# Optimization experiments

Measured on AMD Instinct MI355X. Metric: run time of the kernel, lower is better.

The kernel has to match this reference:

```python
import jax, jax.numpy as jnp
import numpy as np

B, G, D, H, L, MLP = 64, 512, 384, 6, 12, 4
DH = D // H
MASK_RATIO = 0.6
KEEP_RATIO = 0.1
PAD_VAL = -1.0
START_VAL = 1.0
POS_HID = 128
NEG = -1e9


def setup_inputs() -> dict:
    key = jax.random.key(0)
    ks = jax.random.split(key, 24)
    s = 0.02
    inp = {
        "x": jax.random.normal(ks[0], (B, G, D), jnp.float32),
        "center_points": jax.random.normal(ks[1], (B, G, 3), jnp.float32),
        "mask_noise": jax.random.uniform(ks[2], (B, G), jnp.float32),
        # pos embedder MLP: 3 -> 128 -> D
        "pos_w1": jax.random.normal(ks[3], (3, POS_HID), jnp.float32) * s,
        "pos_b1": jnp.zeros((POS_HID,), jnp.float32),
        "pos_w2": jax.random.normal(ks[4], (POS_HID, D), jnp.float32) * s,
        "pos_b2": jnp.zeros((D,), jnp.float32),
        # stacked per-layer transformer params
        "ln1_w": jnp.ones((L, D), jnp.float32),
        "ln1_b": jnp.zeros((L, D), jnp.float32),
        "qkv_w": jax.random.normal(ks[5], (L, D, 3 * D), jnp.float32) * s,
        "qkv_b": jnp.zeros((L, 3 * D), jnp.float32),
        "proj_w": jax.random.normal(ks[6], (L, D, D), jnp.float32) * s,
        "proj_b": jnp.zeros((L, D), jnp.float32),
        "ln2_w": jnp.ones((L, D), jnp.float32),
        "ln2_b": jnp.zeros((L, D), jnp.float32),
        "fc1_w": jax.random.normal(ks[7], (L, D, MLP * D), jnp.float32) * s,
        "fc1_b": jnp.zeros((L, MLP * D), jnp.float32),
        "fc2_w": jax.random.normal(ks[8], (L, MLP * D, D), jnp.float32) * s,
        "fc2_b": jnp.zeros((L, D), jnp.float32),
        # final LayerNorm
        "norm_w": jnp.ones((D,), jnp.float32),
        "norm_b": jnp.zeros((D,), jnp.float32),
    }
    return inp


def _layer_norm(h, w, b, eps=1e-5):
    mu = jnp.mean(h, axis=-1, keepdims=True)
    var = jnp.mean(jnp.square(h - mu), axis=-1, keepdims=True)
    return (h - mu) * jax.lax.rsqrt(var + eps) * w + b


def _random_mask(center, noise):
    # padding tokens: all coords equal PAD_VAL
    pad = jnp.all(center == PAD_VAL, axis=-1)                      # [B, G] bool
    if MASK_RATIO == 0:
        return jnp.zeros(pad.shape, bool), pad
    n = (G - jnp.sum(pad.astype(jnp.int32), axis=-1))              # non-padding count
    k = (n.astype(jnp.float32) * KEEP_RATIO).astype(jnp.int32)     # kept-first tokens
    m = ((n - k).astype(jnp.float32) * MASK_RATIO).astype(jnp.int32)
    M = jnp.max(m)
    j = jnp.arange(G)[None, :]
    # shuffle region [k, n): pick m random slots (uniform subset via rank of noise)
    region = (j >= k[:, None]) & (j < n[:, None])
    u = jnp.where(region, noise, jnp.inf)
    rank = jnp.argsort(jnp.argsort(u, axis=-1), axis=-1)
    shuf = (rank < m[:, None]) & region
    # tail of ones: positions [n, n + M - m)
    tail = (j >= n[:, None]) & (j < (n + M - m)[:, None])
    return shuf | tail, pad


def _attention(h, qw, qb, pw, pb, bias):
    qkv = (h @ qw + qb).reshape(B, G, 3, H, DH).transpose(2, 0, 3, 1, 4)
    q, k, v = qkv[0], qkv[1], qkv[2]                               # [B, H, G, DH]
    s = jnp.einsum('bhqd,bhkd->bhqk', q, k) * (DH ** -0.5) + bias
    a = jax.nn.softmax(s, axis=-1)
    o = jnp.einsum('bhqk,bhkd->bhqd', a, v).transpose(0, 2, 1, 3).reshape(B, G, D)
    return o @ pw + pb


def _forward(x, center_points, mask_noise,
             pos_w1, pos_b1, pos_w2, pos_b2,
             ln1_w, ln1_b, qkv_w, qkv_b, proj_w, proj_b,
             ln2_w, ln2_b, fc1_w, fc1_b, fc2_w, fc2_b,
             norm_w, norm_b):
    # shift right + start token
    start = jnp.full((B, 1, D), START_VAL, x.dtype)
    x = jnp.concatenate([start, x[:, :-1, :]], axis=1)
    # positional embedding of shifted centers + start-token pos
    pos = jax.nn.gelu(center_points[:, :-1, :] @ pos_w1 + pos_b1, approximate=False) @ pos_w2 + pos_b2
    pos = jnp.concatenate([jnp.full((B, 1, D), START_VAL, x.dtype), pos], axis=1)
    # causal | (random column mask & ~eye) attention mask
    triu = jnp.triu(jnp.ones((G, G), bool), 1)
    rand_mask, pad = _random_mask(center_points, mask_noise)
    eye = jnp.eye(G, dtype=bool)
    attn_mask = triu[None, :, :] | (rand_mask[:, None, :] & ~eye[None, :, :])   # [B, G, G]
    bias = jnp.where(attn_mask | pad[:, None, :], NEG, 0.0)[:, None, :, :]      # [B,1,G,G]

    def block(h, p):
        l1w, l1b, qw, qb, pw, pb, l2w, l2b, f1w, f1b, f2w, f2b = p
        h = h + pos
        h = h + _attention(_layer_norm(h, l1w, l1b), qw, qb, pw, pb, bias)
        h = h + (jax.nn.gelu(_layer_norm(h, l2w, l2b) @ f1w + f1b, approximate=False) @ f2w + f2b)
        return h, None

    x, _ = jax.lax.scan(block, x, (ln1_w, ln1_b, qkv_w, qkv_b, proj_w, proj_b,
                                   ln2_w, ln2_b, fc1_w, fc1_b, fc2_w, fc2_b))
    x = _layer_norm(x, norm_w, norm_b)
    return x, pad, attn_mask


def reference(x, center_points, mask_noise,
              pos_w1, pos_b1, pos_w2, pos_b2,
              ln1_w, ln1_b, qkv_w, qkv_b, proj_w, proj_b,
              ln2_w, ln2_b, fc1_w, fc1_b, fc2_w, fc2_b,
              norm_w, norm_b):
    out, pad, attn_mask = _forward(x, center_points, mask_noise,
                                   pos_w1, pos_b1, pos_w2, pos_b2,
                                   ln1_w, ln1_b, qkv_w, qkv_b, proj_w, proj_b,
                                   ln2_w, ln2_b, fc1_w, fc1_b, fc2_w, fc2_b,
                                   norm_w, norm_b)
    # torch repeat_interleave over heads -> [B*H, G, G]
    return out, pad, jnp.repeat(attn_mask, H, axis=0)
```

## Files before the change

kernel.cpp:

```cpp
#include <hip/hip_runtime.h>
#include <math.h>

typedef _Float16 f16;
typedef f16 f16x8 __attribute__((ext_vector_type(8)));
typedef f16 f16v2 __attribute__((ext_vector_type(2)));
typedef float f32x4 __attribute__((ext_vector_type(4)));

#define NB 64
#define NG 512
#define ND 384
#define NH 6
#define NL 12
#define NDH 64
#define BG (NB * NG)
#define BGD (BG * ND)

#define OFF_WQKV   0
#define OFF_WPROJ  2654208
#define OFF_WFC1   3538944
#define OFF_WFC2   7077888
#define OFF_FLAGS  10616832
#define OFF_NKM    10625024
#define OFF_MMAX   10625216
#define OFF_POS    10625280
#define OFF_HID    23208192
#define OFF_Y      25305344
#define OFF_YBIG   31596800
#define OFF_QB     56762624
#define OFF_KB     63054080
#define OFF_VT     69345536
#define OFF_OB     75636992
#define OFF_W2T    81928448
#define OFF_HB     81953024

typedef __attribute__((address_space(3))) void lds_t;
typedef const __attribute__((address_space(1))) void gmem_t;
__device__ __forceinline__ void gload16(const void* g, void* l)
{
    __builtin_amdgcn_global_load_lds((gmem_t*)g, (lds_t*)l, 16, 0, 0);
}

__global__ __launch_bounds__(256)
void transpose_kernel(const float* __restrict__ src, f16* __restrict__ dst,
                      int K, int N)
{
    __shared__ float tile[32][33];
    const int l = blockIdx.z;
    const float* S = src + (size_t)l * K * N;
    f16* D = dst + (size_t)l * K * N;
    const int n0 = blockIdx.x * 32, k0 = blockIdx.y * 32;
    const int tx = threadIdx.x, ty = threadIdx.y;
#pragma unroll
    for (int i = 0; i < 32; i += 8)
        tile[ty + i][tx] = S[(size_t)(k0 + ty + i) * N + n0 + tx];
    __syncthreads();
#pragma unroll
    for (int i = 0; i < 32; i += 8)
        D[(size_t)(n0 + ty + i) * K + k0 + tx] = (f16)tile[tx][ty + i];
}

__global__ __launch_bounds__(256)
void dpos_a(const float* cen, const float* w1, const float* b1, f16* hid)
{
    const int idx = blockIdx.x * 256 + threadIdx.x;
    if (idx >= BG * 128) return;
    const int t = idx >> 7, k = idx & 127;
    const int g = t & (NG - 1);
    if (g == 0) { hid[idx] = (f16)0.f; return; }
    const float* c = cen + (size_t)(t - 1) * 3;
    const float hv = c[0] * w1[k] + c[1] * w1[128 + k] + c[2] * w1[256 + k] + b1[k];
    hid[idx] = (f16)(0.5f * hv * (1.0f + erff(hv * 0.70710678118654752f)));
}

__global__ __launch_bounds__(384)
void pos_fix(float* pos)
{
    const int b = blockIdx.x;
    pos[((size_t)b * NG) * ND + threadIdx.x] = 1.0f;
}

__global__ __launch_bounds__(512)
void dmask_a(const float* cen, float* pad_out, int* nkm)
{
    const int b = blockIdx.x, j = threadIdx.x;
    const float* c = cen + ((size_t)b * NG + j) * 3;
    const bool pad = (c[0] == -1.f) && (c[1] == -1.f) && (c[2] == -1.f);
    pad_out[b * NG + j] = pad ? 1.f : 0.f;
    if (j == 0) {
        int cnt = 0;
        for (int i = 0; i < NG; i++) {
            const float* ci = cen + ((size_t)b * NG + i) * 3;
            cnt += (ci[0] == -1.f && ci[1] == -1.f && ci[2] == -1.f) ? 1 : 0;
        }
        const int n = NG - cnt;
        const int k = (int)((float)n * 0.1f);
        const int m = (int)((float)(n - k) * 0.6f);
        nkm[b * 3] = n; nkm[b * 3 + 1] = k; nkm[b * 3 + 2] = m;
    }
}

__global__ void dmask_m(const int* nkm, int* Mmax)
{
    if (threadIdx.x == 0 && blockIdx.x == 0) {
        int M = 0;
        for (int b = 0; b < NB; b++) M = max(M, nkm[b * 3 + 2]);
        *Mmax = M;
    }
}

__global__ __launch_bounds__(512)
void dmask_b(const float* cen, const float* noi, const int* nkm,
             const int* Mmax, unsigned char* flags)
{
    const int b = blockIdx.x, j = threadIdx.x;
    const int n = nkm[b * 3], k = nkm[b * 3 + 1], m = nkm[b * 3 + 2];
    const int M = *Mmax;
    const float nz = noi[b * NG + j];
    const bool inreg = (j >= k) && (j < n);
    bool shuf = false;
    if (inreg) {
        int cnt = 0;
        for (int i = 0; i < NG; i++) {
            if (i < k || i >= n) continue;
            const float ui = noi[b * NG + i];
            cnt += (ui < nz) || (ui == nz && i < j);
        }
        shuf = cnt < m;
    }
    const float* c = cen + ((size_t)b * NG + j) * 3;
    const bool pad = (c[0] == -1.f) && (c[1] == -1.f) && (c[2] == -1.f);
    const bool tail = (j >= n) && (j < n + M - m);
    flags[b * NG + j] = (unsigned char)(((shuf | tail) ? 1 : 0) | (pad ? 2 : 0));
}

__global__ __launch_bounds__(512)
void flags_rep_kernel(const unsigned char* flags, float* mo)
{
    const int bq = blockIdx.x;
    const int b = bq >> 9, q = bq & (NG - 1);
    const int j = threadIdx.x;
    mo[(((size_t)(b * NH) * NG + q) * NG) + j] = (float)flags[b * NG + j];
}

__global__ __launch_bounds__(512)
void mask_out_kernel(float* mo)
{
    const int bq = blockIdx.x;
    const int b = bq >> 9, q = bq & (NG - 1);
    const int j = threadIdx.x;
    const unsigned char f =
        (unsigned char)mo[(((size_t)(b * NH) * NG + q) * NG) + j];
    const float val = ((q < j) || ((f & 1) && (q != j))) ? 1.0f : 0.0f;
#pragma unroll
    for (int h = 0; h < NH; h++)
        mo[(((size_t)(b * NH + h) * NG + q) * NG) + j] = val;
}

__global__ __launch_bounds__(256)
void h0_kernel(const float* x, const float* pos, f16* h)
{
    const size_t i = (size_t)blockIdx.x * 256 + threadIdx.x;
    const int g = (int)((i / ND) & (NG - 1));
    const float xv = x[(g == 0) ? i : (i - ND)];
    const float base = (g == 0) ? 1.0f : xv;
    h[i] = (f16)(base + pos[i]);
}

template<int MODE>
__global__ __launch_bounds__(256)
void lnb_kernel(const f16* __restrict__ h,
                const float* __restrict__ w, const float* __restrict__ bb,
                f16* __restrict__ y16, float* __restrict__ y32)
{
    __shared__ float red[4][64];
    const int wid = threadIdx.x >> 6;
    const int lane = threadIdx.x & 63;
    const int t = blockIdx.x * 4 + wid;
    const size_t base = (size_t)t * ND + lane;
    float v[6];
    float s = 0.f;
#pragma unroll
    for (int i = 0; i < 6; i++) {
        const float xv = (float)h[base + i * 64];
        v[i] = xv; s += xv;
    }
    red[wid][lane] = s;
    __syncthreads();
    for (int st = 32; st > 0; st >>= 1) {
        if (lane < st) red[wid][lane] += red[wid][lane + st];
        __syncthreads();
    }
    const float mu = red[wid][0] * (1.f / ND);
    float vs = 0.f;
#pragma unroll
    for (int i = 0; i < 6; i++) { const float d = v[i] - mu; vs += d * d; }
    __syncthreads();
    red[wid][lane] = vs;
    __syncthreads();
    for (int st = 32; st > 0; st >>= 1) {
        if (lane < st) red[wid][lane] += red[wid][lane + st];
        __syncthreads();
    }
    const float rstd = rsqrtf(red[wid][0] * (1.f / ND) + 1e-5f);
#pragma unroll
    for (int i = 0; i < 6; i++) {
        const float o = (v[i] - mu) * rstd * w[lane + i * 64] + bb[lane + i * 64];
        if constexpr (MODE == 2) y32[base + i * 64] = o;
        else                     y16[base + i * 64] = (f16)o;
    }
}

template<int MODE>
__global__ __launch_bounds__(256)
void gemm_kernel(const f16* __restrict__ A, const f16* __restrict__ Bt,
                 const float* __restrict__ bias, int K, int NT,
                 f16* __restrict__ hres,
                 float* __restrict__ out32, f16* __restrict__ out16,
                 f16* __restrict__ Qo, f16* __restrict__ Ko, f16* __restrict__ Vo)
{
    __shared__ f16 sA[128 * 64];
    __shared__ f16 sB[128 * 64];
    const int tid = threadIdx.x;
    const int w = tid >> 6, lane = tid & 63;
    const int lr = lane & 15, lg = lane >> 4;
    const int wm = w >> 1, wn = w & 1;
    const int N = NT * 128;

    const int nwg = gridDim.x;
    const int chunk = nwg >> 3;
    const int flat = (blockIdx.x & 7) * chunk + (blockIdx.x >> 3);
    const int m0 = (flat / NT) * 128;
    const int n0 = (flat % NT) * 128;

    f32x4 acc[4][4];
#pragma unroll
    for (int mf = 0; mf < 4; mf++)
#pragma unroll
        for (int nf = 0; nf < 4; nf++)
            acc[mf][nf] = (f32x4){0.f, 0.f, 0.f, 0.f};

    const int srow0 = w * 8 + (lane >> 3);
    const int scolB = (lane & 7) * 16;

    for (int k0 = 0; k0 < K; k0 += 64) {
        __syncthreads();
#pragma unroll
        for (int i = 0; i < 4; i++) {
            const int row = i * 32 + srow0;
            const int colB = scolB ^ ((row & 7) << 4);
            const char* ga = (const char*)(A + (size_t)(m0 + row) * K + k0) + colB;
            const char* gb = (const char*)(Bt + (size_t)(n0 + row) * K + k0) + colB;
            gload16(ga, (char*)sA + row * 128 + scolB);
            gload16(gb, (char*)sB + row * 128 + scolB);
        }
        __syncthreads();
#pragma unroll
        for (int kk = 0; kk < 64; kk += 32) {
            f16x8 af[4], bf[4];
#pragma unroll
            for (int mf = 0; mf < 4; mf++) {
                const int r = wm * 64 + mf * 16 + lr;
                const int cb = ((kk + lg * 8) * 2) ^ ((r & 7) << 4);
                af[mf] = *(const f16x8*)((const char*)sA + r * 128 + cb);
            }
#pragma unroll
            for (int nf = 0; nf < 4; nf++) {
                const int r = wn * 64 + nf * 16 + lr;
                const int cb = ((kk + lg * 8) * 2) ^ ((r & 7) << 4);
                bf[nf] = *(const f16x8*)((const char*)sB + r * 128 + cb);
            }
#pragma unroll
            for (int mf = 0; mf < 4; mf++)
#pragma unroll
                for (int nf = 0; nf < 4; nf++)
                    acc[mf][nf] = __builtin_amdgcn_mfma_f32_16x16x32_f16(
                        af[mf], bf[nf], acc[mf][nf], 0, 0, 0);
        }
    }

#pragma unroll
    for (int mf = 0; mf < 4; mf++) {
#pragma unroll
        for (int nf = 0; nf < 4; nf++) {
            const int n_g = n0 + wn * 64 + nf * 16 + lr;
            const float bv = bias[n_g];
#pragma unroll
            for (int r = 0; r < 4; r++) {
                const int m_g = m0 + wm * 64 + mf * 16 + lg * 4 + r;
                const float v = acc[mf][nf][r] + bv;
                const size_t oidx = (size_t)m_g * N + n_g;
                if constexpr (MODE == 1) {
                    hres[oidx] = (f16)((float)hres[oidx] + v);
                } else if constexpr (MODE == 2) {
                    const float ge = 0.5f * v * (1.0f + erff(v * 0.70710678118654752f));
                    out16[oidx] = (f16)ge;
                } else if constexpr (MODE == 3) {
                    out32[oidx] = v;
                } else {
                    const int which = n_g / ND;
                    const int rem = n_g - which * ND;
                    const int hh = rem >> 6, dh = rem & 63;
                    const int bb2 = m_g >> 9, gg = m_g & (NG - 1);
                    if (which == 0)
                        Qo[((size_t)(bb2 * NH + hh) * NG + gg) * NDH + dh] = (f16)v;
                    else if (which == 1)
                        Ko[((size_t)(bb2 * NH + hh) * NG + gg) * NDH + dh] = (f16)v;
                    else
                        Vo[((size_t)(bb2 * NH + hh) * NDH + dh) * NG + gg] = (f16)v;
                }
            }
        }
    }
}

template<int ADDPOS>
__global__ __launch_bounds__(512)
void gemmln_kernel(const f16* __restrict__ A, const f16* __restrict__ Bt,
                   const float* __restrict__ bias, int K,
                   f16* __restrict__ hres, const float* __restrict__ posadd,
                   const float* __restrict__ lw, const float* __restrict__ lb,
                   f16* __restrict__ Y)
{
    __shared__ f16 sA[128 * 64];
    __shared__ f16 sB[384 * 64];
    __shared__ float part[2][128][2];
    const int tid = threadIdx.x;
    const int w = tid >> 6, lane = tid & 63;
    const int lr = lane & 15, lg = lane >> 4;
    const int wm = w >> 2, wn = w & 3;
    const int vm = w >> 1, vn = w & 1;

    const int nwg = gridDim.x;
    const int chunk = nwg >> 3;
    const int m0 = ((blockIdx.x & 7) * chunk + (blockIdx.x >> 3)) * 128;
    (void)wm; (void)wn;

    f32x4 acc[2][12];
#pragma unroll
    for (int mf = 0; mf < 2; mf++)
#pragma unroll
        for (int nf = 0; nf < 12; nf++)
            acc[mf][nf] = (f32x4){0.f, 0.f, 0.f, 0.f};

    const int srowA = tid >> 3;
    const int scolB = (tid & 7) * 16;

    for (int k0 = 0; k0 < K; k0 += 64) {
        __syncthreads();
#pragma unroll
        for (int i = 0; i < 2; i++) {
            const int row = i * 64 + srowA;
            const int colB = scolB ^ ((row & 7) << 4);
            gload16((const char*)(A + (size_t)(m0 + row) * K + k0) + colB,
                    (char*)sA + row * 128 + scolB);
        }
#pragma unroll
        for (int i = 0; i < 6; i++) {
            const int row = i * 64 + srowA;
            const int colB = scolB ^ ((row & 7) << 4);
            gload16((const char*)(Bt + (size_t)row * K + k0) + colB,
                    (char*)sB + row * 128 + scolB);
        }
        __syncthreads();
#pragma unroll
        for (int kk = 0; kk < 64; kk += 32) {
            f16x8 af[2];
#pragma unroll
            for (int mf = 0; mf < 2; mf++) {
                const int r = vm * 32 + mf * 16 + lr;
                const int cb = ((kk + lg * 8) * 2) ^ ((r & 7) << 4);
                af[mf] = *(const f16x8*)((const char*)sA + r * 128 + cb);
            }
#pragma unroll
            for (int half = 0; half < 2; half++) {
                f16x8 bf[6];
#pragma unroll
                for (int j = 0; j < 6; j++) {
                    const int nf = half * 6 + j;
                    const int r = vn * 192 + nf * 16 + lr;
                    const int cb = ((kk + lg * 8) * 2) ^ ((r & 7) << 4);
                    bf[j] = *(const f16x8*)((const char*)sB + r * 128 + cb);
                }
#pragma unroll
                for (int mf = 0; mf < 2; mf++)
#pragma unroll
                    for (int j = 0; j < 6; j++)
                        acc[mf][half * 6 + j] = __builtin_amdgcn_mfma_f32_16x16x32_f16(
                            af[mf], bf[j], acc[mf][half * 6 + j], 0, 0, 0);
            }
        }
    }

    f16v2 hn[2][12][2];
    float rs[2][4], rq[2][4];
#pragma unroll
    for (int mf = 0; mf < 2; mf++)
#pragma unroll
        for (int r = 0; r < 4; r++) { rs[mf][r] = 0.f; rq[mf][r] = 0.f; }

#pragma unroll
    for (int mf = 0; mf < 2; mf++) {
#pragma unroll
        for (int nf = 0; nf < 12; nf++) {
            const int col = vn * 192 + nf * 16 + lr;
            const float bv = bias[col];
#pragma unroll
            for (int r = 0; r < 4; r++) {
                const int row_g = m0 + vm * 32 + mf * 16 + lg * 4 + r;
                const size_t oidx = (size_t)row_g * ND + col;
                float hv = (float)hres[oidx] + acc[mf][nf][r] + bv;
                if constexpr (ADDPOS) hv += posadd[oidx];
                const f16 hf = (f16)hv;
                hn[mf][nf][r >> 1][r & 1] = hf;
                const float hff = (float)hf;
                rs[mf][r] += hff;
                rq[mf][r] += hff * hff;
            }
        }
    }
#pragma unroll
    for (int mf = 0; mf < 2; mf++)
#pragma unroll
        for (int r = 0; r < 4; r++) {
#pragma unroll
            for (int off = 1; off < 16; off <<= 1) {
                rs[mf][r] += __shfl_xor(rs[mf][r], off);
                rq[mf][r] += __shfl_xor(rq[mf][r], off);
            }
        }
    if (lr == 0) {
#pragma unroll
        for (int mf = 0; mf < 2; mf++)
#pragma unroll
            for (int r = 0; r < 4; r++) {
                const int rl = vm * 32 + mf * 16 + lg * 4 + r;
                part[vn][rl][0] = rs[mf][r];
                part[vn][rl][1] = rq[mf][r];
            }
    }
    __syncthreads();

    float mus[2][4], rstds[2][4];
#pragma unroll
    for (int mf = 0; mf < 2; mf++)
#pragma unroll
        for (int r = 0; r < 4; r++) {
            const int rl = vm * 32 + mf * 16 + lg * 4 + r;
            const float s = part[0][rl][0] + part[1][rl][0];
            const float q = part[0][rl][1] + part[1][rl][1];
            const float mu = s * (1.f / ND);
            const float var = q * (1.f / ND) - mu * mu;
            mus[mf][r] = mu;
            rstds[mf][r] = rsqrtf(var + 1e-5f);
        }

#pragma unroll
    for (int mf = 0; mf < 2; mf++) {
#pragma unroll
        for (int nf = 0; nf < 12; nf++) {
            const int col = vn * 192 + nf * 16 + lr;
            const float wl = lw[col];
            const float bl = lb[col];
#pragma unroll
            for (int r = 0; r < 4; r++) {
                const int row_g = m0 + vm * 32 + mf * 16 + lg * 4 + r;
                const size_t oidx = (size_t)row_g * ND + col;
                const f16 hf = hn[mf][nf][r >> 1][r & 1];
                hres[oidx] = hf;
                const float o = ((float)hf - mus[mf][r]) * rstds[mf][r] * wl + bl;
                Y[oidx] = (f16)o;
            }
        }
    }
}

__global__ __launch_bounds__(256)
void attn_kernel(const f16* __restrict__ Q, const f16* __restrict__ Kt,
                 const f16* __restrict__ V, const unsigned char* __restrict__ flags,
                 f16* __restrict__ O)
{
    __shared__ f16 sQ[128][72];
    __shared__ f16 sK[64][72];
    __shared__ f16 sV[64][72];
    __shared__ f16 sP[4][16][72];
    const int tid = threadIdx.x;
    const int w = tid >> 6, lane = tid & 63;
    const int lr = lane & 15, lg = lane >> 4;
    const int q0 = blockIdx.x * 128;
    const int bh = blockIdx.y;
    const int b = bh / NH, hh = bh - b * NH;
    const f16* Qg = Q + ((size_t)bh * NG + q0) * NDH;
    const f16* Kg = Kt + (size_t)bh * NG * NDH;
    const f16* Vg = V + (size_t)bh * NDH * NG;
    const unsigned char* fl = flags + b * NG;

#pragma unroll
    for (int i = 0; i < 4; i++) {
        const int c = tid + i * 256;
        const int r = c >> 3, cc = (c & 7) * 8;
        *(f16x8*)&sQ[r][cc] = *(const f16x8*)(Qg + r * NDH + cc);
    }
    __syncthreads();
    f16x8 aq[2][2];
#pragma unroll
    for (int hf = 0; hf < 2; hf++) {
        aq[hf][0] = *(const f16x8*)&sQ[hf * 64 + w * 16 + lr][lg * 8];
        aq[hf][1] = *(const f16x8*)&sQ[hf * 64 + w * 16 + lr][32 + lg * 8];
    }

    float m_run[2][4], l_run[2][4];
    f32x4 o[2][4];
#pragma unroll
    for (int hf = 0; hf < 2; hf++)
#pragma unroll
        for (int r = 0; r < 4; r++) {
            m_run[hf][r] = -INFINITY; l_run[hf][r] = 0.f;
            o[hf][r] = (f32x4){0.f, 0.f, 0.f, 0.f};
        }

    const int ntile = 2 * blockIdx.x + 2;
    for (int jt = 0; jt < ntile; jt++) {
        const int j0 = jt * 64;
        __syncthreads();
#pragma unroll
        for (int i = 0; i < 2; i++) {
            const int c = tid + i * 256;
            const int r = c >> 3, cc = (c & 7) * 8;
            *(f16x8*)&sK[r][cc] = *(const f16x8*)(Kg + (size_t)(j0 + r) * NDH + cc);
            *(f16x8*)&sV[r][cc] = *(const f16x8*)(Vg + (size_t)r * NG + j0 + cc);
        }
        __syncthreads();

#pragma unroll
        for (int hf = 0; hf < 2; hf++) {
            if (jt >= ntile - 1 + hf) continue;
            f32x4 s[4];
#pragma unroll
            for (int nf = 0; nf < 4; nf++) s[nf] = (f32x4){0.f, 0.f, 0.f, 0.f};
#pragma unroll
            for (int kf = 0; kf < 2; kf++) {
#pragma unroll
                for (int nf = 0; nf < 4; nf++) {
                    f16x8 bk = *(const f16x8*)&sK[nf * 16 + lr][kf * 32 + lg * 8];
                    s[nf] = __builtin_amdgcn_mfma_f32_16x16x32_f16(aq[hf][kf], bk, s[nf], 0, 0, 0);
                }
            }
#pragma unroll
            for (int nf = 0; nf < 4; nf++) {
                const int j_g = j0 + nf * 16 + lr;
                const unsigned char f = fl[j_g];
#pragma unroll
                for (int r = 0; r < 4; r++) {
                    const int q_g = q0 + hf * 64 + w * 16 + lg * 4 + r;
                    const bool masked = (q_g < j_g) || (f & 2) || ((f & 1) && (j_g != q_g));
                    s[nf][r] = s[nf][r] * 0.125f + (masked ? -1e9f : 0.f);
                }
            }
#pragma unroll
            for (int r = 0; r < 4; r++) {
                float mx = fmaxf(fmaxf(s[0][r], s[1][r]), fmaxf(s[2][r], s[3][r]));
#pragma unroll
                for (int off = 1; off < 16; off <<= 1) mx = fmaxf(mx, __shfl_xor(mx, off));
                const float nm = fmaxf(m_run[hf][r], mx);
                const float sc = __expf(m_run[hf][r] - nm);
                m_run[hf][r] = nm;
                l_run[hf][r] *= sc;
#pragma unroll
                for (int nf = 0; nf < 4; nf++) o[hf][nf][r] *= sc;
                float ls = 0.f;
#pragma unroll
                for (int nf = 0; nf < 4; nf++) {
                    const float p = __expf(s[nf][r] - nm);
                    ls += p;
                    sP[w][lg * 4 + r][nf * 16 + lr] = (f16)p;
                }
                l_run[hf][r] += ls;
            }
#pragma unroll
            for (int kf = 0; kf < 2; kf++) {
                f16x8 ap = *(const f16x8*)&sP[w][lr][kf * 32 + lg * 8];
#pragma unroll
                for (int nf = 0; nf < 4; nf++) {
                    f16x8 bv = *(const f16x8*)&sV[nf * 16 + lr][kf * 32 + lg * 8];
                    o[hf][nf] = __builtin_amdgcn_mfma_f32_16x16x32_f16(ap, bv, o[hf][nf], 0, 0, 0);
                }
            }
        }
    }

#pragma unroll
    for (int hf = 0; hf < 2; hf++) {
        float inv[4];
#pragma unroll
        for (int r = 0; r < 4; r++) {
            float l = l_run[hf][r];
#pragma unroll
            for (int off = 1; off < 16; off <<= 1) l += __shfl_xor(l, off);
            inv[r] = 1.f / l;
        }
#pragma unroll
        for (int nf = 0; nf < 4; nf++) {
#pragma unroll
            for (int r = 0; r < 4; r++) {
                const int q_g = q0 + hf * 64 + w * 16 + lg * 4 + r;
                const int dh = nf * 16 + lr;
                O[((size_t)(b * NG + q_g)) * ND + hh * NDH + dh] = (f16)(o[hf][nf][r] * inv[r]);
            }
        }
    }
}

extern "C" void kernel_launch(void* const* d_in, const int* in_sizes, int n_in,
                              void* d_out, int out_size, void* d_ws, size_t ws_size,
                              hipStream_t stream)
{
    (void)d_ws; (void)ws_size;

    static const int exp_sizes[21] = {
        12582912, 98304, 32768,
        384, 128, 49152, 384,
        4608, 4608,
        5308416, 13824,
        1769472, 4608,
        4608, 4608,
        7077888, 18432,
        7077888, 4608,
        384, 384
    };
    if (n_in != 21 || out_size != 113278976) return;
    for (int i = 0; i < 21; i++) if (in_sizes[i] != exp_sizes[i]) return;

    const float* x    = (const float*)d_in[0];
    const float* cen  = (const float*)d_in[1];
    const float* noi  = (const float*)d_in[2];
    const float* pw1  = (const float*)d_in[3];
    const float* pb1  = (const float*)d_in[4];
    const float* pw2  = (const float*)d_in[5];
    const float* pb2  = (const float*)d_in[6];
    const float* ln1w = (const float*)d_in[7];
    const float* ln1b = (const float*)d_in[8];
    const float* qkvw = (const float*)d_in[9];
    const float* qkvb = (const float*)d_in[10];
    const float* projw= (const float*)d_in[11];
    const float* projb= (const float*)d_in[12];
    const float* ln2w = (const float*)d_in[13];
    const float* ln2b = (const float*)d_in[14];
    const float* fc1w = (const float*)d_in[15];
    const float* fc1b = (const float*)d_in[16];
    const float* fc2w = (const float*)d_in[17];
    const float* fc2b = (const float*)d_in[18];
    const float* nw   = (const float*)d_in[19];
    const float* nb   = (const float*)d_in[20];

    float* out0    = (float*)d_out;
    float* pad_out = out0 + BGD;
    float* R       = pad_out + BG;

    f16* WqkvT  = (f16*)(R + OFF_WQKV);
    f16* WprojT = (f16*)(R + OFF_WPROJ);
    f16* Wfc1T  = (f16*)(R + OFF_WFC1);
    f16* Wfc2T  = (f16*)(R + OFF_WFC2);
    unsigned char* flags = (unsigned char*)(R + OFF_FLAGS);
    int* nkm  = (int*)(R + OFF_NKM);
    int* Mmax = (int*)(R + OFF_MMAX);
    float* POS = R + OFF_POS;
    f16* HID   = (f16*)(R + OFF_HID);
    f16* Y     = (f16*)(R + OFF_Y);
    f16* Ybig  = (f16*)(R + OFF_YBIG);
    f16* Qb    = (f16*)(R + OFF_QB);
    f16* Kb    = (f16*)(R + OFF_KB);
    f16* Vt    = (f16*)(R + OFF_VT);
    f16* Ob    = (f16*)(R + OFF_OB);
    f16* W2T   = (f16*)(R + OFF_W2T);
    f16* Hb    = (f16*)(R + OFF_HB);

    dim3 tb(32, 8);
    transpose_kernel<<<dim3(36, 12, NL), tb, 0, stream>>>(qkvw, WqkvT, 384, 1152);
    transpose_kernel<<<dim3(12, 12, NL), tb, 0, stream>>>(projw, WprojT, 384, 384);
    transpose_kernel<<<dim3(48, 12, NL), tb, 0, stream>>>(fc1w, Wfc1T, 384, 1536);
    transpose_kernel<<<dim3(12, 48, NL), tb, 0, stream>>>(fc2w, Wfc2T, 1536, 384);
    transpose_kernel<<<dim3(12, 4, 1),  tb, 0, stream>>>(pw2, W2T, 128, 384);

    dmask_a<<<NB, 512, 0, stream>>>(cen, pad_out, nkm);
    dmask_m<<<1, 64, 0, stream>>>(nkm, Mmax);
    dmask_b<<<NB, 512, 0, stream>>>(cen, noi, nkm, Mmax, flags);
    dpos_a<<<BG * 128 / 256, 256, 0, stream>>>(cen, pw1, pb1, HID);
    gemm_kernel<3><<<768, 256, 0, stream>>>(HID, W2T, pb2, 128, 3,
                                            nullptr, POS, nullptr,
                                            nullptr, nullptr, nullptr);
    pos_fix<<<NB, 384, 0, stream>>>(POS);
    h0_kernel<<<BGD / 256, 256, 0, stream>>>(x, POS, Hb);

    lnb_kernel<1><<<BG / 4, 256, 0, stream>>>(Hb, ln1w, ln1b, Y, nullptr);

    for (int l = 0; l < NL; l++) {
        gemm_kernel<0><<<2304, 256, 0, stream>>>(Y, WqkvT + (size_t)l * 442368,
                                                 qkvb + l * 1152, 384, 9,
                                                 nullptr, nullptr, nullptr,
                                                 Qb, Kb, Vt);
        attn_kernel<<<dim3(4, NB * NH), 256, 0, stream>>>(Qb, Kb, Vt, flags, Ob);
        gemmln_kernel<0><<<256, 512, 0, stream>>>(Ob, WprojT + (size_t)l * 147456,
                                                  projb + l * ND, 384,
                                                  Hb, nullptr,
                                                  ln2w + l * ND, ln2b + l * ND, Y);
        gemm_kernel<2><<<3072, 256, 0, stream>>>(Y, Wfc1T + (size_t)l * 589824,
                                                 fc1b + l * 1536, 384, 12,
                                                 nullptr, nullptr, Ybig,
                                                 nullptr, nullptr, nullptr);
        if (l < NL - 1) {
            gemmln_kernel<1><<<256, 512, 0, stream>>>(Ybig, Wfc2T + (size_t)l * 589824,
                                                      fc2b + l * ND, 1536,
                                                      Hb, POS,
                                                      ln1w + (l + 1) * ND, ln1b + (l + 1) * ND, Y);
        } else {
            gemm_kernel<1><<<768, 256, 0, stream>>>(Ybig, Wfc2T + (size_t)l * 589824,
                                                    fc2b + l * ND, 1536, 3,
                                                    Hb, nullptr, nullptr,
                                                    nullptr, nullptr, nullptr);
        }
    }

    lnb_kernel<2><<<BG / 4, 256, 0, stream>>>(Hb, nw, nb, nullptr, out0);
    flags_rep_kernel<<<BG, 512, 0, stream>>>(flags, R);
    mask_out_kernel<<<BG, 512, 0, stream>>>(R);
}
```

Before: 4.962 ms.

## Shrink attention query tile and read K/V directly; store positional embedding in fp16

The attention kernel now handles 64 queries per block instead of 128, launching twice as many blocks. It drops the shared-memory staging of Q, K and V and loads MFMA operands straight from global memory, removing the block barriers and the uneven two-half causal work split. Separately, the positional-embedding buffer is stored in fp16 rather than fp32, halving its write and its re-read in every fc2+LayerNorm epilogue. The trade-offs are lost K/V reuse through LDS, which means more global and L2 traffic from uncoalesced fragment loads, and lower precision on the positional add.

```diff
diff --git a/kernel.cpp b/kernel.cpp
--- a/kernel.cpp
+++ b/kernel.cpp
@@ -73,10 +73,10 @@
 }
 
 __global__ __launch_bounds__(384)
-void pos_fix(float* pos)
+void pos_fix(f16* pos)
 {
     const int b = blockIdx.x;
-    pos[((size_t)b * NG) * ND + threadIdx.x] = 1.0f;
+    pos[((size_t)b * NG) * ND + threadIdx.x] = (f16)1.0f;
 }
 
 __global__ __launch_bounds__(512)
@@ -157,13 +157,13 @@
 }
 
 __global__ __launch_bounds__(256)
-void h0_kernel(const float* x, const float* pos, f16* h)
+void h0_kernel(const float* x, const f16* pos, f16* h)
 {
     const size_t i = (size_t)blockIdx.x * 256 + threadIdx.x;
     const int g = (int)((i / ND) & (NG - 1));
     const float xv = x[(g == 0) ? i : (i - ND)];
     const float base = (g == 0) ? 1.0f : xv;
-    h[i] = (f16)(base + pos[i]);
+    h[i] = (f16)(base + (float)pos[i]);
 }
 
 template<int MODE>
@@ -214,8 +214,7 @@
 __global__ __launch_bounds__(256)
 void gemm_kernel(const f16* __restrict__ A, const f16* __restrict__ Bt,
                  const float* __restrict__ bias, int K, int NT,
-                 f16* __restrict__ hres,
-                 float* __restrict__ out32, f16* __restrict__ out16,
+                 f16* __restrict__ hres, f16* __restrict__ out16,
                  f16* __restrict__ Qo, f16* __restrict__ Ko, f16* __restrict__ Vo)
 {
     __shared__ f16 sA[128 * 64];
@@ -295,7 +294,7 @@
                     const float ge = 0.5f * v * (1.0f + erff(v * 0.70710678118654752f));
                     out16[oidx] = (f16)ge;
                 } else if constexpr (MODE == 3) {
-                    out32[oidx] = v;
+                    out16[oidx] = (f16)v;
                 } else {
                     const int which = n_g / ND;
                     const int rem = n_g - which * ND;
@@ -317,7 +316,7 @@
 __global__ __launch_bounds__(512)
 void gemmln_kernel(const f16* __restrict__ A, const f16* __restrict__ Bt,
                    const float* __restrict__ bias, int K,
-                   f16* __restrict__ hres, const float* __restrict__ posadd,
+                   f16* __restrict__ hres, const f16* __restrict__ posadd,
                    const float* __restrict__ lw, const float* __restrict__ lb,
                    f16* __restrict__ Y)
 {
@@ -327,13 +326,11 @@
     const int tid = threadIdx.x;
     const int w = tid >> 6, lane = tid & 63;
     const int lr = lane & 15, lg = lane >> 4;
-    const int wm = w >> 2, wn = w & 3;
     const int vm = w >> 1, vn = w & 1;
 
     const int nwg = gridDim.x;
     const int chunk = nwg >> 3;
     const int m0 = ((blockIdx.x & 7) * chunk + (blockIdx.x >> 3)) * 128;
-    (void)wm; (void)wn;
 
     f32x4 acc[2][12];
 #pragma unroll
@@ -409,7 +406,7 @@
                 const int row_g = m0 + vm * 32 + mf * 16 + lg * 4 + r;
                 const size_t oidx = (size_t)row_g * ND + col;
                 float hv = (float)hres[oidx] + acc[mf][nf][r] + bv;
-                if constexpr (ADDPOS) hv += posadd[oidx];
+                if constexpr (ADDPOS) hv += (float)posadd[oidx];
                 const f16 hf = (f16)hv;
                 hn[mf][nf][r >> 1][r & 1] = hf;
                 const float hff = (float)hf;
@@ -479,133 +476,104 @@
                  const f16* __restrict__ V, const unsigned char* __restrict__ flags,
                  f16* __restrict__ O)
 {
-    __shared__ f16 sQ[128][72];
-    __shared__ f16 sK[64][72];
-    __shared__ f16 sV[64][72];
     __shared__ f16 sP[4][16][72];
     const int tid = threadIdx.x;
     const int w = tid >> 6, lane = tid & 63;
     const int lr = lane & 15, lg = lane >> 4;
-    const int q0 = blockIdx.x * 128;
+    const int q0 = blockIdx.x * 64;
     const int bh = blockIdx.y;
     const int b = bh / NH, hh = bh - b * NH;
-    const f16* Qg = Q + ((size_t)bh * NG + q0) * NDH;
+    const f16* Qg = Q + (size_t)bh * NG * NDH;
     const f16* Kg = Kt + (size_t)bh * NG * NDH;
     const f16* Vg = V + (size_t)bh * NDH * NG;
     const unsigned char* fl = flags + b * NG;
 
-#pragma unroll
-    for (int i = 0; i < 4; i++) {
-        const int c = tid + i * 256;
-        const int r = c >> 3, cc = (c & 7) * 8;
-        *(f16x8*)&sQ[r][cc] = *(const f16x8*)(Qg + r * NDH + cc);
-    }
-    __syncthreads();
-    f16x8 aq[2][2];
-#pragma unroll
-    for (int hf = 0; hf < 2; hf++) {
-        aq[hf][0] = *(const f16x8*)&sQ[hf * 64 + w * 16 + lr][lg * 8];
-        aq[hf][1] = *(const f16x8*)&sQ[hf * 64 + w * 16 + lr][32 + lg * 8];
-    }
-
-    float m_run[2][4], l_run[2][4];
-    f32x4 o[2][4];
-#pragma unroll
-    for (int hf = 0; hf < 2; hf++)
-#pragma unroll
-        for (int r = 0; r < 4; r++) {
-            m_run[hf][r] = -INFINITY; l_run[hf][r] = 0.f;
-            o[hf][r] = (f32x4){0.f, 0.f, 0.f, 0.f};
-        }
-
-    const int ntile = 2 * blockIdx.x + 2;
+    const int qrow = q0 + w * 16 + lr;
+    f16x8 aq[2];
+    aq[0] = *(const f16x8*)(Qg + (size_t)qrow * NDH + lg * 8);
+    aq[1] = *(const f16x8*)(Qg + (size_t)qrow * NDH + 32 + lg * 8);
+
+    float m_run[4], l_run[4];
+    f32x4 o[4];
+#pragma unroll
+    for (int r = 0; r < 4; r++) { m_run[r] = -INFINITY; l_run[r] = 0.f; }
+#pragma unroll
+    for (int nf = 0; nf < 4; nf++) o[nf] = (f32x4){0.f, 0.f, 0.f, 0.f};
+
+    const int ntile = blockIdx.x + 1;
     for (int jt = 0; jt < ntile; jt++) {
         const int j0 = jt * 64;
-        __syncthreads();
-#pragma unroll
-        for (int i = 0; i < 2; i++) {
-            const int c = tid + i * 256;
-            const int r = c >> 3, cc = (c & 7) * 8;
-            *(f16x8*)&sK[r][cc] = *(const f16x8*)(Kg + (size_t)(j0 + r) * NDH + cc);
-            *(f16x8*)&sV[r][cc] = *(const f16x8*)(Vg + (size_t)r * NG + j0 + cc);
-        }
-        __syncthreads();
-
-#pragma unroll
-        for (int hf = 0; hf < 2; hf++) {
-            if (jt >= ntile - 1 + hf) continue;
-            f32x4 s[4];
-#pragma unroll
-            for (int nf = 0; nf < 4; nf++) s[nf] = (f32x4){0.f, 0.f, 0.f, 0.f};
-#pragma unroll
-            for (int kf = 0; kf < 2; kf++) {
-#pragma unroll
-                for (int nf = 0; nf < 4; nf++) {
-                    f16x8 bk = *(const f16x8*)&sK[nf * 16 + lr][kf * 32 + lg * 8];
-                    s[nf] = __builtin_amdgcn_mfma_f32_16x16x32_f16(aq[hf][kf], bk, s[nf], 0, 0, 0);
-                }
-            }
+
+        f32x4 s[4];
+#pragma unroll
+        for (int nf = 0; nf < 4; nf++) s[nf] = (f32x4){0.f, 0.f, 0.f, 0.f};
+#pragma unroll
+        for (int kf = 0; kf < 2; kf++) {
 #pragma unroll
             for (int nf = 0; nf < 4; nf++) {
-                const int j_g = j0 + nf * 16 + lr;
-                const unsigned char f = fl[j_g];
-#pragma unroll
-                for (int r = 0; r < 4; r++) {
-                    const int q_g = q0 + hf * 64 + w * 16 + lg * 4 + r;
-                    const bool masked = (q_g < j_g) || (f & 2) || ((f & 1) && (j_g != q_g));
-                    s[nf][r] = s[nf][r] * 0.125f + (masked ? -1e9f : 0.f);
-                }
-            }
+                f16x8 bk = *(const f16x8*)(Kg + (size_t)(j0 + nf * 16 + lr) * NDH
+                                           + kf * 32 + lg * 8);
+                s[nf] = __builtin_amdgcn_mfma_f32_16x16x32_f16(aq[kf], bk, s[nf], 0, 0, 0);
+            }
+        }
+#pragma unroll
+        for (int nf = 0; nf < 4; nf++) {
+            const int j_g = j0 + nf * 16 + lr;
+            const unsigned char f = fl[j_g];
 #pragma unroll
             for (int r = 0; r < 4; r++) {
-                float mx = fmaxf(fmaxf(s[0][r], s[1][r]), fmaxf(s[2][r], s[3][r]));
-#pragma unroll
-                for (int off = 1; off < 16; off <<= 1) mx = fmaxf(mx, __shfl_xor(mx, off));
-                const float nm = fmaxf(m_run[hf][r], mx);
-                const float sc = __expf(m_run[hf][r] - nm);
-                m_run[hf][r] = nm;
-                l_run[hf][r] *= sc;
-#pragma unroll
-                for (int nf = 0; nf < 4; nf++) o[hf][nf][r] *= sc;
-                float ls = 0.f;
-#pragma unroll
-                for (int nf = 0; nf < 4; nf++) {
-                    const float p = __expf(s[nf][r] - nm);
-                    ls += p;
-                    sP[w][lg * 4 + r][nf * 16 + lr] = (f16)p;
-                }
-                l_run[hf][r] += ls;
-            }
-#pragma unroll
-            for (int kf = 0; kf < 2; kf++) {
-                f16x8 ap = *(const f16x8*)&sP[w][lr][kf * 32 + lg * 8];
-#pragma unroll
-                for (int nf = 0; nf < 4; nf++) {
-                    f16x8 bv = *(const f16x8*)&sV[nf * 16 + lr][kf * 32 + lg * 8];
-                    o[hf][nf] = __builtin_amdgcn_mfma_f32_16x16x32_f16(ap, bv, o[hf][nf], 0, 0, 0);
-                }
-            }
-        }
-    }
-
-#pragma unroll
-    for (int hf = 0; hf < 2; hf++) {
-        float inv[4];
+                const int q_g = q0 + w * 16 + lg * 4 + r;
+                const bool masked = (q_g < j_g) || (f & 2) || ((f & 1) && (j_g != q_g));
+                s[nf][r] = s[nf][r] * 0.125f + (masked ? -1e9f : 0.f);
+            }
+        }
 #pragma unroll
         for (int r = 0; r < 4; r++) {
-            float l = l_run[hf][r];
-#pragma unroll
-            for (int off = 1; off < 16; off <<= 1) l += __shfl_xor(l, off);
-            inv[r] = 1.f / l;
-        }
-#pragma unroll
-        for (int nf = 0; nf < 4; nf++) {
-#pragma unroll
-            for (int r = 0; r < 4; r++) {
-                const int q_g = q0 + hf * 64 + w * 16 + lg * 4 + r;
-                const int dh = nf * 16 + lr;
-                O[((size_t)(b * NG + q_g)) * ND + hh * NDH + dh] = (f16)(o[hf][nf][r] * inv[r]);
-            }
+            float mx = fmaxf(fmaxf(s[0][r], s[1][r]), fmaxf(s[2][r], s[3][r]));
+#pragma unroll
+            for (int off = 1; off < 16; off <<= 1) mx = fmaxf(mx, __shfl_xor(mx, off));
+            const float nm = fmaxf(m_run[r], mx);
+            const float sc = __expf(m_run[r] - nm);
+            m_run[r] = nm;
+            l_run[r] *= sc;
+#pragma unroll
+            for (int nf = 0; nf < 4; nf++) o[nf][r] *= sc;
+            float ls = 0.f;
+#pragma unroll
+            for (int nf = 0; nf < 4; nf++) {
+                const float p = __expf(s[nf][r] - nm);
+                ls += p;
+                sP[w][lg * 4 + r][nf * 16 + lr] = (f16)p;
+            }
+            l_run[r] += ls;
+        }
+#pragma unroll
+        for (int kf = 0; kf < 2; kf++) {
+            f16x8 ap = *(const f16x8*)&sP[w][lr][kf * 32 + lg * 8];
+#pragma unroll
+            for (int nf = 0; nf < 4; nf++) {
+                f16x8 bv = *(const f16x8*)(Vg + (size_t)(nf * 16 + lr) * NG
+                                           + j0 + kf * 32 + lg * 8);
+                o[nf] = __builtin_amdgcn_mfma_f32_16x16x32_f16(ap, bv, o[nf], 0, 0, 0);
+            }
+        }
+    }
+
+    float inv[4];
+#pragma unroll
+    for (int r = 0; r < 4; r++) {
+        float l = l_run[r];
+#pragma unroll
+        for (int off = 1; off < 16; off <<= 1) l += __shfl_xor(l, off);
+        inv[r] = 1.f / l;
+    }
+#pragma unroll
+    for (int nf = 0; nf < 4; nf++) {
+#pragma unroll
+        for (int r = 0; r < 4; r++) {
+            const int q_g = q0 + w * 16 + lg * 4 + r;
+            const int dh = nf * 16 + lr;
+            O[((size_t)(b * NG + q_g)) * ND + hh * NDH + dh] = (f16)(o[nf][r] * inv[r]);
         }
     }
 }
@@ -663,7 +631,7 @@
     unsigned char* flags = (unsigned char*)(R + OFF_FLAGS);
     int* nkm  = (int*)(R + OFF_NKM);
     int* Mmax = (int*)(R + OFF_MMAX);
-    float* POS = R + OFF_POS;
+    f16* POS   = (f16*)(R + OFF_POS);
     f16* HID   = (f16*)(R + OFF_HID);
     f16* Y     = (f16*)(R + OFF_Y);
     f16* Ybig  = (f16*)(R + OFF_YBIG);
@@ -686,7 +654,7 @@
     dmask_b<<<NB, 512, 0, stream>>>(cen, noi, nkm, Mmax, flags);
     dpos_a<<<BG * 128 / 256, 256, 0, stream>>>(cen, pw1, pb1, HID);
     gemm_kernel<3><<<768, 256, 0, stream>>>(HID, W2T, pb2, 128, 3,
-                                            nullptr, POS, nullptr,
+                                            nullptr, POS,
                                             nullptr, nullptr, nullptr);
     pos_fix<<<NB, 384, 0, stream>>>(POS);
     h0_kernel<<<BGD / 256, 256, 0, stream>>>(x, POS, Hb);
@@ -696,16 +664,16 @@
     for (int l = 0; l < NL; l++) {
         gemm_kernel<0><<<2304, 256, 0, stream>>>(Y, WqkvT + (size_t)l * 442368,
                                                  qkvb + l * 1152, 384, 9,
-                                                 nullptr, nullptr, nullptr,
+                                                 nullptr, nullptr,
                                                  Qb, Kb, Vt);
-        attn_kernel<<<dim3(4, NB * NH), 256, 0, stream>>>(Qb, Kb, Vt, flags, Ob);
+        attn_kernel<<<dim3(8, NB * NH), 256, 0, stream>>>(Qb, Kb, Vt, flags, Ob);
         gemmln_kernel<0><<<256, 512, 0, stream>>>(Ob, WprojT + (size_t)l * 147456,
                                                   projb + l * ND, 384,
                                                   Hb, nullptr,
                                                   ln2w + l * ND, ln2b + l * ND, Y);
         gemm_kernel<2><<<3072, 256, 0, stream>>>(Y, Wfc1T + (size_t)l * 589824,
                                                  fc1b + l * 1536, 384, 12,
-                                                 nullptr, nullptr, Ybig,
+                                                 nullptr, Ybig,
                                                  nullptr, nullptr, nullptr);
         if (l < NL - 1) {
             gemmln_kernel<1><<<256, 512, 0, stream>>>(Ybig, Wfc2T + (size_t)l * 589824,
@@ -715,7 +683,7 @@
         } else {
             gemm_kernel<1><<<768, 256, 0, stream>>>(Ybig, Wfc2T + (size_t)l * 589824,
                                                     fc2b + l * ND, 1536, 3,
-                                                    Hb, nullptr, nullptr,
+                                                    Hb, nullptr,
                                                     nullptr, nullptr, nullptr);
         }
     }
```

After: 5.619 ms. 13.2% more time.
